# Kernel tuning notes

Measured on AMD Instinct MI355X. Metric: run time of the kernel, lower is better.

The kernel has to match this reference:

```python
import jax, jax.numpy as jnp
import numpy as np

# Static graph-batch configuration (equal-size graphs so per-graph top-k is static)
B = 256          # number of graphs in the batch
N = 400          # nodes per graph
D = 256          # in_dim
DEG = 32         # average degree
E = B * N * DEG  # total edges
RATIO = 0.5
K = int(np.ceil(RATIO * N))  # nodes kept per graph by mytopk
NT = B * N


def setup_inputs() -> dict:
    key = jax.random.key(0)
    k1, k2, k3, k4 = jax.random.split(key, 4)
    feature = jax.random.normal(k1, (NT, D), dtype=jnp.float32)
    W = jax.random.normal(k2, (D, 1), dtype=jnp.float32) * (1.0 / np.sqrt(D))
    b = jnp.zeros((1,), dtype=jnp.float32)
    # edges stay within each graph: global id = graph_offset + local id
    g = jnp.repeat(jnp.arange(B, dtype=jnp.int32), N * DEG)  # [E] graph id per edge
    src = g * N + jax.random.randint(k3, (E,), 0, N, dtype=jnp.int32)
    dst = g * N + jax.random.randint(k4, (E,), 0, N, dtype=jnp.int32)
    return {"feature": feature, "W": W, "b": b, "src": src, "dst": dst}


def _forward(feature, W, b, src, dst):
    # --- GraphConv(in_dim, 1), norm='both' (dgl): h = D_in^-1/2 A D_out^-1/2 (X W) + b
    ones_e = jnp.ones((E,), dtype=feature.dtype)
    deg_out = jax.ops.segment_sum(ones_e, src, num_segments=NT)
    deg_in = jax.ops.segment_sum(ones_e, dst, num_segments=NT)
    norm_out = jnp.maximum(deg_out, 1.0) ** -0.5  # dgl clamps degree to min 1
    norm_in = jnp.maximum(deg_in, 1.0) ** -0.5
    h = (feature @ W) * norm_out[:, None]                      # [NT,1]
    agg = jax.ops.segment_sum(h[src], dst, num_segments=NT)    # [NT,1]
    score = (agg * norm_in[:, None] + b)[:, 0]                 # [NT]

    # --- mytopk: per-graph top-k node selection by score (descending)
    score2d = score.reshape(B, N)
    _, idx = jax.lax.top_k(score2d, K)                         # [B,K] local ids
    offsets = (jnp.arange(B, dtype=jnp.int32) * N)[:, None]
    perm = (idx.astype(jnp.int32) + offsets).reshape(-1)       # [B*K] global ids

    # complement nodes (mask trick in the original): ascending order per graph
    sel = jnp.zeros((NT,), dtype=bool).at[perm].set(True)
    sel2d = sel.reshape(B, N).astype(jnp.int32)
    order = jnp.argsort(sel2d, axis=1, stable=True)[:, : N - K]  # unselected first
    perm_com = (order.astype(jnp.int32) + offsets).reshape(-1)   # [B*(N-K)]

    # --- gated feature gathers
    feature_dis = feature[perm] * jnp.tanh(score[perm])[:, None]
    feature_com = feature[perm_com] * jnp.tanh(score[perm_com])[:, None]

    # --- subgraph structure as static-shape edge masks (dgl.node_subgraph keeps
    #     edges whose both endpoints are selected)
    e_dis_mask = sel[src] & sel[dst]
    e_com_mask = (~sel[src]) & (~sel[dst])

    score_soft = jax.nn.softmax(score, axis=0)  # Softmax(dim=0) over all nodes
    return feature_dis, feature_com, perm, perm_com, score_soft, e_dis_mask, e_com_mask


def reference(feature, W, b, src, dst):
    return _forward(feature, W, b, src, dst)
```

## Files before the change

### kernel.cpp

```cpp
#include <hip/hip_runtime.h>
#include <math.h>

#define B_    256
#define N_    400
#define D_    256
#define EPG_  12800
#define E_    3276800
#define NT_   102400
#define K_    200
#define NKC_  200

#define O_FDIS 0
#define O_FCOM 13107200
#define O_PERM 26214400
#define O_PCOM 26265600
#define O_SOFT 26316800
#define O_EDIS 26419200
#define O_ECOM 29696000

#define NEG_INF (-3.402823466e38f)

typedef float nfv4 __attribute__((ext_vector_type(4)));

static __device__ __forceinline__ void nt_store4(float4* p, float4 v) {
    nfv4 x; x.x = v.x; x.y = v.y; x.z = v.z; x.w = v.w;
    __builtin_nontemporal_store(x, (nfv4*)p);
}

__global__ __launch_bounds__(1024) void k_graph(const float* __restrict__ feat,
                                                const float* __restrict__ W,
                                                const int* __restrict__ src,
                                                const int* __restrict__ dst,
                                                const float* __restrict__ bp,
                                                float* __restrict__ score,
                                                float* __restrict__ pm,
                                                float* __restrict__ ps,
                                                int* __restrict__ orow,
                                                float* __restrict__ out) {
    __shared__ float hl[N_], scl[N_];
    __shared__ int   ho[N_], hi[N_], smask[N_];
    const int g = blockIdx.x, tid = threadIdx.x;
    const int nbase = g * N_, ebase = g * EPG_;
    const int wave = tid >> 6, lane = tid & 63;

    if (tid < N_) { ho[tid] = 0; hi[tid] = 0; scl[tid] = 0.0f; }
    __syncthreads();

    const int4* s4 = (const int4*)(src + ebase);
    const int4* d4 = (const int4*)(dst + ebase);

    if (wave < 12) {
        const float4 w4 = ((const float4*)W)[lane];
        const float4* fb = (const float4*)feat + (size_t)nbase * 64;
        for (int r = wave; r < N_; r += 24) {
            const int r2 = r + 12;
            float4 a0 = fb[(size_t)r * 64 + lane];
            float4 a1 = (r2 < N_) ? fb[(size_t)r2 * 64 + lane]
                                  : make_float4(0.f, 0.f, 0.f, 0.f);
            float d0 = a0.x*w4.x + a0.y*w4.y + a0.z*w4.z + a0.w*w4.w;
            float d1 = a1.x*w4.x + a1.y*w4.y + a1.z*w4.z + a1.w*w4.w;
            #pragma unroll
            for (int off = 32; off > 0; off >>= 1) {
                d0 += __shfl_down(d0, off, 64);
                d1 += __shfl_down(d1, off, 64);
            }
            if (lane == 0) {
                hl[r] = d0;
                if (r2 < N_) hl[r2] = d1;
            }
        }
    } else {
        for (int i = tid - 768; i < EPG_ / 4; i += 256) {
            int4 s = s4[i]; int4 d = d4[i];
            atomicAdd(&ho[s.x - nbase], 1);
            atomicAdd(&ho[s.y - nbase], 1);
            atomicAdd(&ho[s.z - nbase], 1);
            atomicAdd(&ho[s.w - nbase], 1);
            atomicAdd(&hi[d.x - nbase], 1);
            atomicAdd(&hi[d.y - nbase], 1);
            atomicAdd(&hi[d.z - nbase], 1);
            atomicAdd(&hi[d.w - nbase], 1);
        }
    }
    __syncthreads();

    if (tid < N_)
        hl[tid] = hl[tid] * (1.0f / sqrtf(fmaxf((float)ho[tid], 1.0f)));
    __syncthreads();

    for (int i = tid; i < EPG_ / 4; i += 1024) {
        int4 s = s4[i]; int4 d = d4[i];
        atomicAdd(&scl[d.x - nbase], hl[s.x - nbase]);
        atomicAdd(&scl[d.y - nbase], hl[s.y - nbase]);
        atomicAdd(&scl[d.z - nbase], hl[s.z - nbase]);
        atomicAdd(&scl[d.w - nbase], hl[s.w - nbase]);
    }
    __syncthreads();

    const float bb = bp[0];
    if (tid < N_) {
        float v = scl[tid] * (1.0f / sqrtf(fmaxf((float)hi[tid], 1.0f))) + bb;
        scl[tid] = v;
        score[nbase + tid] = v;
    }
    __syncthreads();

    if (tid < N_) {
        const float v = scl[tid];
        int r = 0;
        for (int j = 0; j < N_; ++j) {
            float u = scl[j];
            r += (u > v) || (u == v && j < tid);
        }
        const int selb = (r < K_) ? 1 : 0;
        smask[tid] = selb;
        if (selb) {
            orow[nbase + tid] = g * K_ + r;
            out[O_PERM + g * K_ + r] = (float)(nbase + tid);
        }
    }
    if (wave == 15) {
        float m = NEG_INF;
        for (int i = lane; i < N_; i += 64) m = fmaxf(m, scl[i]);
        #pragma unroll
        for (int o = 32; o > 0; o >>= 1) m = fmaxf(m, __shfl_xor(m, o, 64));
        float s = 0.0f;
        for (int i = lane; i < N_; i += 64) s += expf(scl[i] - m);
        #pragma unroll
        for (int o = 32; o > 0; o >>= 1) s += __shfl_xor(s, o, 64);
        if (lane == 0) { pm[g] = m; ps[g] = s; }
    }
    __syncthreads();

    if (tid < N_ && !smask[tid]) {
        int pos = 0;
        for (int u = 0; u < tid; ++u) pos += (smask[u] == 0);
        orow[nbase + tid] = B_ * K_ + g * NKC_ + pos;
        out[O_PCOM + g * NKC_ + pos] = (float)(nbase + tid);
    }

    float4* mdis = (float4*)(out + O_EDIS) + g * (EPG_ / 4);
    float4* mcom = (float4*)(out + O_ECOM) + g * (EPG_ / 4);
    for (int i = tid; i < EPG_ / 4; i += 1024) {
        int4 s = s4[i]; int4 d = d4[i];
        int a0 = smask[s.x - nbase], a1 = smask[s.y - nbase];
        int a2 = smask[s.z - nbase], a3 = smask[s.w - nbase];
        int b0 = smask[d.x - nbase], b1 = smask[d.y - nbase];
        int b2 = smask[d.z - nbase], b3 = smask[d.w - nbase];
        float4 vdis, vcom;
        vdis.x = (a0 & b0) ? 1.0f : 0.0f;  vcom.x = (a0 | b0) ? 0.0f : 1.0f;
        vdis.y = (a1 & b1) ? 1.0f : 0.0f;  vcom.y = (a1 | b1) ? 0.0f : 1.0f;
        vdis.z = (a2 & b2) ? 1.0f : 0.0f;  vcom.z = (a2 | b2) ? 0.0f : 1.0f;
        vdis.w = (a3 & b3) ? 1.0f : 0.0f;  vcom.w = (a3 | b3) ? 0.0f : 1.0f;
        nt_store4(&mdis[i], vdis);
        nt_store4(&mcom[i], vcom);
    }
}

__global__ __launch_bounds__(256) void k_soft_comb(const float* pm, const float* ps, float* red2) {
    __shared__ float rm[256], rs[256];
    int tid = threadIdx.x;
    float m = pm[tid];
    rm[tid] = m; __syncthreads();
    for (int o = 128; o > 0; o >>= 1) { if (tid < o) rm[tid] = fmaxf(rm[tid], rm[tid + o]); __syncthreads(); }
    float M = rm[0]; __syncthreads();
    rs[tid] = ps[tid] * expf(m - M); __syncthreads();
    for (int o = 128; o > 0; o >>= 1) { if (tid < o) rs[tid] += rs[tid + o]; __syncthreads(); }
    if (tid == 0) { red2[0] = M; red2[1] = rs[0]; }
}

__global__ __launch_bounds__(256) void k_gather(const float* __restrict__ feat,
                                                const float* __restrict__ score,
                                                const int* __restrict__ orow,
                                                const float* __restrict__ red2,
                                                float* __restrict__ out) {
    const int gw   = (blockIdx.x * 256 + threadIdx.x) >> 6;
    const int lane = threadIdx.x & 63;
    const int n0 = gw * 4;
    const float4* fb = (const float4*)feat;
    float4 v0 = fb[(size_t)(n0    ) * 64 + lane];
    float4 v1 = fb[(size_t)(n0 + 1) * 64 + lane];
    float4 v2 = fb[(size_t)(n0 + 2) * 64 + lane];
    float4 v3 = fb[(size_t)(n0 + 3) * 64 + lane];
    float s0 = score[n0], s1 = score[n0 + 1], s2 = score[n0 + 2], s3 = score[n0 + 3];
    int   r0 = orow[n0],  r1 = orow[n0 + 1],  r2 = orow[n0 + 2],  r3 = orow[n0 + 3];
    float t0 = tanhf(s0), t1 = tanhf(s1), t2 = tanhf(s2), t3 = tanhf(s3);
    v0.x *= t0; v0.y *= t0; v0.z *= t0; v0.w *= t0;
    v1.x *= t1; v1.y *= t1; v1.z *= t1; v1.w *= t1;
    v2.x *= t2; v2.y *= t2; v2.z *= t2; v2.w *= t2;
    v3.x *= t3; v3.y *= t3; v3.z *= t3; v3.w *= t3;
    nt_store4(((float4*)(out + (size_t)r0 * D_)) + lane, v0);
    nt_store4(((float4*)(out + (size_t)r1 * D_)) + lane, v1);
    nt_store4(((float4*)(out + (size_t)r2 * D_)) + lane, v2);
    nt_store4(((float4*)(out + (size_t)r3 * D_)) + lane, v3);
    if (lane == 0) {
        float M = red2[0], S = red2[1];
        out[O_SOFT + n0    ] = expf(s0 - M) / S;
        out[O_SOFT + n0 + 1] = expf(s1 - M) / S;
        out[O_SOFT + n0 + 2] = expf(s2 - M) / S;
        out[O_SOFT + n0 + 3] = expf(s3 - M) / S;
    }
}

extern "C" void kernel_launch(void* const* d_in, const int* in_sizes, int n_in,
                              void* d_out, int out_size, void* d_ws, size_t ws_size,
                              hipStream_t stream) {
    const float* feat = (const float*)d_in[0];
    const float* W    = (const float*)d_in[1];
    const float* bp   = (const float*)d_in[2];
    const int*   src  = (const int*)d_in[3];
    const int*   dst  = (const int*)d_in[4];
    float* out = (float*)d_out;

    char* ws = (char*)d_ws;
    float* score = (float*)(ws + 0);
    int*   orow  = (int*)  (ws + 409600);
    float* pm    = (float*)(ws + 819200);
    float* ps    = (float*)(ws + 820224);
    float* red2  = (float*)(ws + 821248);

    k_graph    <<<B_,      1024, 0, stream>>>(feat, W, src, dst, bp,
                                              score, pm, ps, orow, out);
    k_soft_comb<<<1,        256, 0, stream>>>(pm, ps, red2);
    k_gather   <<<NT_ / 16, 256, 0, stream>>>(feat, score, orow, red2, out);
}
```

Before: 285.7 us.

## Fuse feature gather into per-graph kernel and speed up rank computation

Moves the gated feature scatter into the per-graph kernel, which reuses shared-memory row maps and tanh values instead of a workspace round trip, and drops the separate gather launch. Rank counting now broadcasts scores through register shuffles, and the complement position is a ballot-popcount prefix rather than a serial loop. The softmax combine is folded into a grid-wide normalisation kernel, and the matvec loop is unrolled to four rows. The cost is that the 26 MB gather now runs on only 256 blocks, which may underuse bandwidth compared with the old wide launch.

```diff
diff --git a/kernel.cpp b/kernel.cpp
--- a/kernel.cpp
+++ b/kernel.cpp
@@ -35,10 +35,14 @@
                                                 float* __restrict__ score,
                                                 float* __restrict__ pm,
                                                 float* __restrict__ ps,
-                                                int* __restrict__ orow,
                                                 float* __restrict__ out) {
     __shared__ float hl[N_], scl[N_];
-    __shared__ int   ho[N_], hi[N_], smask[N_];
+    __shared__ int   ho[N_], hi[N_];
+    __shared__ unsigned long long bmask[7];
+    int*   orow_l = ho;
+    int*   smask  = hi;
+    float* tl     = hl;
+
     const int g = blockIdx.x, tid = threadIdx.x;
     const int nbase = g * N_, ebase = g * EPG_;
     const int wave = tid >> 6, lane = tid & 63;
@@ -48,25 +52,32 @@
 
     const int4* s4 = (const int4*)(src + ebase);
     const int4* d4 = (const int4*)(dst + ebase);
+    const float4* fb = (const float4*)feat + (size_t)nbase * 64;
 
     if (wave < 12) {
         const float4 w4 = ((const float4*)W)[lane];
-        const float4* fb = (const float4*)feat + (size_t)nbase * 64;
-        for (int r = wave; r < N_; r += 24) {
-            const int r2 = r + 12;
+        for (int r = wave; r < N_; r += 48) {
+            const int r1 = r + 12, r2 = r + 24, r3 = r + 36;
             float4 a0 = fb[(size_t)r * 64 + lane];
-            float4 a1 = (r2 < N_) ? fb[(size_t)r2 * 64 + lane]
-                                  : make_float4(0.f, 0.f, 0.f, 0.f);
+            float4 a1 = (r1 < N_) ? fb[(size_t)r1 * 64 + lane] : make_float4(0.f,0.f,0.f,0.f);
+            float4 a2 = (r2 < N_) ? fb[(size_t)r2 * 64 + lane] : make_float4(0.f,0.f,0.f,0.f);
+            float4 a3 = (r3 < N_) ? fb[(size_t)r3 * 64 + lane] : make_float4(0.f,0.f,0.f,0.f);
             float d0 = a0.x*w4.x + a0.y*w4.y + a0.z*w4.z + a0.w*w4.w;
             float d1 = a1.x*w4.x + a1.y*w4.y + a1.z*w4.z + a1.w*w4.w;
+            float d2 = a2.x*w4.x + a2.y*w4.y + a2.z*w4.z + a2.w*w4.w;
+            float d3 = a3.x*w4.x + a3.y*w4.y + a3.z*w4.z + a3.w*w4.w;
             #pragma unroll
             for (int off = 32; off > 0; off >>= 1) {
                 d0 += __shfl_down(d0, off, 64);
                 d1 += __shfl_down(d1, off, 64);
+                d2 += __shfl_down(d2, off, 64);
+                d3 += __shfl_down(d3, off, 64);
             }
             if (lane == 0) {
                 hl[r] = d0;
-                if (r2 < N_) hl[r2] = d1;
+                if (r1 < N_) hl[r1] = d1;
+                if (r2 < N_) hl[r2] = d2;
+                if (r3 < N_) hl[r3] = d3;
             }
         }
     } else {
@@ -102,22 +113,37 @@
         float v = scl[tid] * (1.0f / sqrtf(fmaxf((float)hi[tid], 1.0f))) + bb;
         scl[tid] = v;
         score[nbase + tid] = v;
-    }
-    __syncthreads();
-
-    if (tid < N_) {
-        const float v = scl[tid];
-        int r = 0;
-        for (int j = 0; j < N_; ++j) {
-            float u = scl[j];
-            r += (u > v) || (u == v && j < tid);
-        }
-        const int selb = (r < K_) ? 1 : 0;
-        smask[tid] = selb;
+        tl[tid] = tanhf(v);
+    }
+    __syncthreads();
+
+    bool selb = false;
+    if (tid < 448) {
+        float sreg[7];
+        #pragma unroll
+        for (int t = 0; t < 7; ++t) {
+            const int j = t * 64 + lane;
+            sreg[t] = (j < N_) ? scl[j] : NEG_INF;
+        }
+        const float v = (tid < N_) ? scl[tid] : NEG_INF;
+        int rnk = 0;
+        #pragma unroll
+        for (int t = 0; t < 7; ++t) {
+            #pragma unroll
+            for (int l2 = 0; l2 < 64; ++l2) {
+                const float u = __shfl(sreg[t], l2, 64);
+                const int j = t * 64 + l2;
+                rnk += ((u > v) || (u == v && j < tid)) ? 1 : 0;
+            }
+        }
+        selb = (tid < N_) && (rnk < K_);
+        if (tid < N_) smask[tid] = selb ? 1 : 0;
         if (selb) {
-            orow[nbase + tid] = g * K_ + r;
-            out[O_PERM + g * K_ + r] = (float)(nbase + tid);
-        }
+            orow_l[tid] = g * K_ + rnk;
+            out[O_PERM + g * K_ + rnk] = (float)(nbase + tid);
+        }
+        unsigned long long bal = __ballot(selb);
+        if (lane == 0) bmask[wave] = bal;
     }
     if (wave == 15) {
         float m = NEG_INF;
@@ -132,12 +158,17 @@
     }
     __syncthreads();
 
-    if (tid < N_ && !smask[tid]) {
-        int pos = 0;
-        for (int u = 0; u < tid; ++u) pos += (smask[u] == 0);
-        orow[nbase + tid] = B_ * K_ + g * NKC_ + pos;
+    if (tid < N_ && !selb) {
+        int nsel = 0;
+        #pragma unroll
+        for (int w = 0; w < 7; ++w)
+            if (w < wave) nsel += (int)__popcll(bmask[w]);
+        nsel += (int)__popcll(bmask[wave] & ((1ull << lane) - 1ull));
+        const int pos = tid - nsel;
+        orow_l[tid] = B_ * K_ + g * NKC_ + pos;
         out[O_PCOM + g * NKC_ + pos] = (float)(nbase + tid);
     }
+    __syncthreads();
 
     float4* mdis = (float4*)(out + O_EDIS) + g * (EPG_ / 4);
     float4* mcom = (float4*)(out + O_ECOM) + g * (EPG_ / 4);
@@ -155,51 +186,55 @@
         nt_store4(&mdis[i], vdis);
         nt_store4(&mcom[i], vcom);
     }
-}
-
-__global__ __launch_bounds__(256) void k_soft_comb(const float* pm, const float* ps, float* red2) {
-    __shared__ float rm[256], rs[256];
-    int tid = threadIdx.x;
-    float m = pm[tid];
-    rm[tid] = m; __syncthreads();
-    for (int o = 128; o > 0; o >>= 1) { if (tid < o) rm[tid] = fmaxf(rm[tid], rm[tid + o]); __syncthreads(); }
-    float M = rm[0]; __syncthreads();
-    rs[tid] = ps[tid] * expf(m - M); __syncthreads();
-    for (int o = 128; o > 0; o >>= 1) { if (tid < o) rs[tid] += rs[tid + o]; __syncthreads(); }
-    if (tid == 0) { red2[0] = M; red2[1] = rs[0]; }
-}
-
-__global__ __launch_bounds__(256) void k_gather(const float* __restrict__ feat,
-                                                const float* __restrict__ score,
-                                                const int* __restrict__ orow,
-                                                const float* __restrict__ red2,
-                                                float* __restrict__ out) {
-    const int gw   = (blockIdx.x * 256 + threadIdx.x) >> 6;
-    const int lane = threadIdx.x & 63;
-    const int n0 = gw * 4;
-    const float4* fb = (const float4*)feat;
-    float4 v0 = fb[(size_t)(n0    ) * 64 + lane];
-    float4 v1 = fb[(size_t)(n0 + 1) * 64 + lane];
-    float4 v2 = fb[(size_t)(n0 + 2) * 64 + lane];
-    float4 v3 = fb[(size_t)(n0 + 3) * 64 + lane];
-    float s0 = score[n0], s1 = score[n0 + 1], s2 = score[n0 + 2], s3 = score[n0 + 3];
-    int   r0 = orow[n0],  r1 = orow[n0 + 1],  r2 = orow[n0 + 2],  r3 = orow[n0 + 3];
-    float t0 = tanhf(s0), t1 = tanhf(s1), t2 = tanhf(s2), t3 = tanhf(s3);
-    v0.x *= t0; v0.y *= t0; v0.z *= t0; v0.w *= t0;
-    v1.x *= t1; v1.y *= t1; v1.z *= t1; v1.w *= t1;
-    v2.x *= t2; v2.y *= t2; v2.z *= t2; v2.w *= t2;
-    v3.x *= t3; v3.y *= t3; v3.z *= t3; v3.w *= t3;
-    nt_store4(((float4*)(out + (size_t)r0 * D_)) + lane, v0);
-    nt_store4(((float4*)(out + (size_t)r1 * D_)) + lane, v1);
-    nt_store4(((float4*)(out + (size_t)r2 * D_)) + lane, v2);
-    nt_store4(((float4*)(out + (size_t)r3 * D_)) + lane, v3);
-    if (lane == 0) {
-        float M = red2[0], S = red2[1];
-        out[O_SOFT + n0    ] = expf(s0 - M) / S;
-        out[O_SOFT + n0 + 1] = expf(s1 - M) / S;
-        out[O_SOFT + n0 + 2] = expf(s2 - M) / S;
-        out[O_SOFT + n0 + 3] = expf(s3 - M) / S;
-    }
+
+    {
+        const int base = wave * 25;
+        for (int u = 0; u < 25; u += 5) {
+            const int n0 = base + u, n1 = n0 + 1, n2 = n0 + 2, n3 = n0 + 3, n4 = n0 + 4;
+            const int r0 = orow_l[n0], r1 = orow_l[n1], r2 = orow_l[n2],
+                      r3 = orow_l[n3], r4 = orow_l[n4];
+            const float t0 = tl[n0], t1 = tl[n1], t2 = tl[n2], t3 = tl[n3], t4 = tl[n4];
+            float4 v0 = fb[(size_t)n0 * 64 + lane];
+            float4 v1 = fb[(size_t)n1 * 64 + lane];
+            float4 v2 = fb[(size_t)n2 * 64 + lane];
+            float4 v3 = fb[(size_t)n3 * 64 + lane];
+            float4 v4 = fb[(size_t)n4 * 64 + lane];
+            v0.x *= t0; v0.y *= t0; v0.z *= t0; v0.w *= t0;
+            v1.x *= t1; v1.y *= t1; v1.z *= t1; v1.w *= t1;
+            v2.x *= t2; v2.y *= t2; v2.z *= t2; v2.w *= t2;
+            v3.x *= t3; v3.y *= t3; v3.z *= t3; v3.w *= t3;
+            v4.x *= t4; v4.y *= t4; v4.z *= t4; v4.w *= t4;
+            nt_store4(((float4*)(out + (size_t)r0 * D_)) + lane, v0);
+            nt_store4(((float4*)(out + (size_t)r1 * D_)) + lane, v1);
+            nt_store4(((float4*)(out + (size_t)r2 * D_)) + lane, v2);
+            nt_store4(((float4*)(out + (size_t)r3 * D_)) + lane, v3);
+            nt_store4(((float4*)(out + (size_t)r4 * D_)) + lane, v4);
+        }
+    }
+}
+
+__global__ __launch_bounds__(256) void k_soft(const float* __restrict__ score,
+                                              const float* __restrict__ pm,
+                                              const float* __restrict__ ps,
+                                              float* __restrict__ out) {
+    __shared__ float sm[4], ss[4];
+    const int tid = threadIdx.x, lane = tid & 63, wv = tid >> 6;
+    float m = pm[tid], s = ps[tid];
+    #pragma unroll
+    for (int o = 32; o > 0; o >>= 1) {
+        float mo = __shfl_xor(m, o, 64);
+        float so = __shfl_xor(s, o, 64);
+        float M2 = fmaxf(m, mo);
+        s = s * expf(m - M2) + so * expf(mo - M2);
+        m = M2;
+    }
+    if (lane == 0) { sm[wv] = m; ss[wv] = s; }
+    __syncthreads();
+    const float M = fmaxf(fmaxf(sm[0], sm[1]), fmaxf(sm[2], sm[3]));
+    const float S = ss[0] * expf(sm[0] - M) + ss[1] * expf(sm[1] - M)
+                  + ss[2] * expf(sm[2] - M) + ss[3] * expf(sm[3] - M);
+    const int n = blockIdx.x * 256 + tid;
+    out[O_SOFT + n] = expf(score[n] - M) / S;
 }
 
 extern "C" void kernel_launch(void* const* d_in, const int* in_sizes, int n_in,
@@ -214,13 +249,10 @@
 
     char* ws = (char*)d_ws;
     float* score = (float*)(ws + 0);
-    int*   orow  = (int*)  (ws + 409600);
-    float* pm    = (float*)(ws + 819200);
-    float* ps    = (float*)(ws + 820224);
-    float* red2  = (float*)(ws + 821248);
-
-    k_graph    <<<B_,      1024, 0, stream>>>(feat, W, src, dst, bp,
-                                              score, pm, ps, orow, out);
-    k_soft_comb<<<1,        256, 0, stream>>>(pm, ps, red2);
-    k_gather   <<<NT_ / 16, 256, 0, stream>>>(feat, score, orow, red2, out);
-}
+    float* pm    = (float*)(ws + 409600);
+    float* ps    = (float*)(ws + 410624);
+
+    k_graph<<<B_,       1024, 0, stream>>>(feat, W, src, dst, bp,
+                                           score, pm, ps, out);
+    k_soft <<<NT_ / 256, 256, 0, stream>>>(score, pm, ps, out);
+}
```

New measurement: 291.1 us. No clear change (+1.9%).
